# Performance work log

Measured on AMD Instinct MI355X. Metric: run time of the kernel, lower is better.

Reference implementation:

```python
import jax, jax.numpy as jnp
import numpy as np

N, E, IN, H, C, L = 40000, 640000, 256, 128, 64, 4
ALPHA, LAMB = 0.5, 1.0


def setup_inputs() -> dict:
    key = jax.random.key(0)
    ks = jax.random.split(key, 8)
    x = jax.random.normal(ks[0], (N, IN), jnp.float32)
    src = jax.random.randint(ks[1], (E,), 0, N, jnp.int32)
    dst = jax.random.randint(ks[2], (E,), 0, N, jnp.int32)
    s_in = 1.0 / np.sqrt(IN)
    s_h = 1.0 / np.sqrt(H)
    fc1_w = jax.random.normal(ks[3], (IN, H), jnp.float32) * s_in
    fc1_b = jnp.zeros((H,), jnp.float32)
    W1 = jax.random.normal(ks[4], (L, H, H), jnp.float32) * s_h   # GCN2Conv weight1 per layer
    W2 = jax.random.normal(ks[5], (L, H, H), jnp.float32) * s_h   # GCN2Conv weight2 (initial-residual proj)
    bgc = jnp.zeros((L, H), jnp.float32)                          # GCN2Conv bias per layer
    fc2_w = jax.random.normal(ks[6], (H, C), jnp.float32) * s_h
    fc2_b = jnp.zeros((C,), jnp.float32)
    return dict(x=x, fc1_w=fc1_w, fc1_b=fc1_b, W1=W1, W2=W2, bgc=bgc,
                fc2_w=fc2_w, fc2_b=fc2_b, src=src, dst=dst)


def reference(x, fc1_w, fc1_b, W1, W2, bgc, fc2_w, fc2_b, src, dst):
    ones = jnp.ones((E,), x.dtype)
    # symmetric 'both' normalization: deg_out^{-1/2} on src side, deg_in^{-1/2} on dst side
    deg_out = jnp.clip(jax.ops.segment_sum(ones, src, num_segments=N), 1.0)
    deg_in = jnp.clip(jax.ops.segment_sum(ones, dst, num_segments=N), 1.0)
    norm_s = (deg_out ** -0.5)[:, None]
    norm_d = (deg_in ** -0.5)[:, None]

    # feature_preprocess: dropout (eval = identity) -> fc1 -> relu
    h0 = jax.nn.relu(x @ fc1_w + fc1_b)          # [N, H]
    h = h0
    for l in range(L):
        beta = float(np.log(LAMB / (l + 1) + 1.0))
        identity = h
        # sparse neighbor aggregation (SpMM via gather + segment_sum)
        agg = jax.ops.segment_sum((h * norm_s)[src], dst, num_segments=N) * norm_d
        feat = (1.0 - ALPHA) * agg               # smoothed features
        f0 = ALPHA * h0                          # initial residual
        rst = (1.0 - beta) * (feat + f0) + beta * (feat @ W1[l] + f0 @ W2[l]) + bgc[l]
        h = jax.nn.relu(rst + identity)          # outer residual + activation (dropout eval = identity)
    return h @ fc2_w + fc2_b                     # [N, C]
```

## Files before the change

kernel.cpp:

```cpp
#include <hip/hip_runtime.h>
#include <math.h>

#define N_NODES 40000
#define N_EDGES 640000
#define IN_F 256
#define H_F 128
#define C_F 64
#define L_LAYERS 4
#define SCAN_BLKS 157

typedef short short8 __attribute__((ext_vector_type(8)));
typedef unsigned short ushort8 __attribute__((ext_vector_type(8)));
typedef float f32x4 __attribute__((ext_vector_type(4)));

__device__ inline short to_bf16(float f) {
    unsigned u = __builtin_bit_cast(unsigned, f);
    unsigned r = (u + 0x7FFFu + ((u >> 16) & 1u)) >> 16;
    return (short)r;
}
__device__ inline float bf16_to_f(unsigned short u) {
    unsigned v = ((unsigned)u) << 16;
    return __builtin_bit_cast(float, v);
}

__device__ inline int block_excl_scan(int v, int* wsum, int* tot) {
    int tid = threadIdx.x;
    int lane = tid & 63, wid = tid >> 6;
    int incl = v;
    #pragma unroll
    for (int off = 1; off < 64; off <<= 1) {
        int t = __shfl_up(incl, off, 64);
        if (lane >= off) incl += t;
    }
    if (lane == 63) wsum[wid] = incl;
    __syncthreads();
    int prefix = 0, total = 0;
    #pragma unroll
    for (int w = 0; w < 4; w++) {
        int s = wsum[w];
        if (w < wid) prefix += s;
        total += s;
    }
    *tot = total;
    return prefix + incl - v;
}

__global__ void prep_w(const float* __restrict__ fc1_w,
                       const float* __restrict__ W1, const float* __restrict__ W2,
                       const float* __restrict__ fc2_w,
                       short* __restrict__ fc1_wT, short* __restrict__ WcatT,
                       short* __restrict__ fc2_wT) {
    int i = blockIdx.x * 256 + threadIdx.x;
    if (i < 128 * 256) {
        int n = i >> 8, k = i & 255;
        fc1_wT[i] = to_bf16(fc1_w[k * H_F + n]);
    }
    if (i < 4 * 128 * 256) {
        int l = i >> 15; int r = i & 32767; int n = r >> 8; int k = r & 255;
        float w = (k < 128) ? W1[l * 16384 + k * H_F + n]
                            : W2[l * 16384 + (k - 128) * H_F + n];
        WcatT[i] = to_bf16(0.5f * w);
    }
    if (i < 64 * 128) {
        int n = i >> 7, k = i & 127;
        fc2_wT[i] = to_bf16(fc2_w[k * C_F + n]);
    }
}

#define CVT8(dstv, p) {                                                         \
    float4 _v0 = *(const float4*)(p); float4 _v1 = *(const float4*)((p) + 4);   \
    dstv[0] = to_bf16(_v0.x); dstv[1] = to_bf16(_v0.y);                         \
    dstv[2] = to_bf16(_v0.z); dstv[3] = to_bf16(_v0.w);                         \
    dstv[4] = to_bf16(_v1.x); dstv[5] = to_bf16(_v1.y);                         \
    dstv[6] = to_bf16(_v1.z); dstv[7] = to_bf16(_v1.w); }

__global__ __launch_bounds__(256) void deg_fc1_fused(const int* __restrict__ src,
                                                     const int* __restrict__ dst,
                                                     int* __restrict__ cnt_out,
                                                     int* __restrict__ cnt_in,
                                                     unsigned short* __restrict__ pos16,
                                                     const float* __restrict__ x,
                                                     const short* __restrict__ wT,
                                                     const float* __restrict__ b,
                                                     unsigned short* __restrict__ h0b) {
    int blk = blockIdx.x;
    if ((blk & 1) == 0) {
        int e0 = (blk >> 1) * 1024 + threadIdx.x * 4;
        int4 s4 = *(const int4*)(src + e0);
        int4 d4 = *(const int4*)(dst + e0);
        pos16[e0 + 0] = (unsigned short)atomicAdd(&cnt_in[d4.x], 1);
        pos16[e0 + 1] = (unsigned short)atomicAdd(&cnt_in[d4.y], 1);
        pos16[e0 + 2] = (unsigned short)atomicAdd(&cnt_in[d4.z], 1);
        pos16[e0 + 3] = (unsigned short)atomicAdd(&cnt_in[d4.w], 1);
        atomicAdd(&cnt_out[s4.x], 1);
        atomicAdd(&cnt_out[s4.y], 1);
        atomicAdd(&cnt_out[s4.z], 1);
        atomicAdd(&cnt_out[s4.w], 1);
        return;
    }
    int bb = blk >> 1;
    int tid = threadIdx.x;
    int wave = tid >> 6, lane = tid & 63;
    int m = lane & 15, quad = lane >> 4;
    int row = bb * 64 + wave * 16 + m;
    const float* xr = x + (size_t)row * IN_F + quad * 8;
    short8 afrag[8];
    #pragma unroll
    for (int ks = 0; ks < 8; ks++) {
        CVT8(afrag[ks], xr + ks * 32);
    }
    #pragma unroll
    for (int c = 0; c < 8; c += 2) {
        f32x4 acc0 = {0.f, 0.f, 0.f, 0.f};
        f32x4 acc1 = {0.f, 0.f, 0.f, 0.f};
        const short* b0p = wT + (size_t)(c * 16 + m) * IN_F + quad * 8;
        const short* b1p = b0p + 16 * IN_F;
        #pragma unroll
        for (int ks = 0; ks < 8; ks++) {
            short8 b0 = *(const short8*)(b0p + ks * 32);
            short8 b1 = *(const short8*)(b1p + ks * 32);
            acc0 = __builtin_amdgcn_mfma_f32_16x16x32_bf16(afrag[ks], b0, acc0, 0, 0, 0);
            acc1 = __builtin_amdgcn_mfma_f32_16x16x32_bf16(afrag[ks], b1, acc1, 0, 0, 0);
        }
        int col0 = c * 16 + m;
        int rbase = bb * 64 + wave * 16 + quad * 4;
        float bg0 = b[col0], bg1 = b[col0 + 16];
        #pragma unroll
        for (int r = 0; r < 4; r++) {
            size_t idx = (size_t)(rbase + r) * H_F + col0;
            float v0 = acc0[r] + bg0;
            float v1 = acc1[r] + bg1;
            v0 = v0 > 0.f ? v0 : 0.f;
            v1 = v1 > 0.f ? v1 : 0.f;
            h0b[idx] = (unsigned short)to_bf16(v0);
            h0b[idx + 16] = (unsigned short)to_bf16(v1);
        }
    }
}

__global__ __launch_bounds__(256) void scan1(const int* __restrict__ cnt_in,
                                             int* __restrict__ row_local,
                                             int* __restrict__ blk_sum) {
    __shared__ int wsum[4];
    int n = blockIdx.x * 256 + threadIdx.x;
    int v = (n < N_NODES) ? cnt_in[n] : 0;
    int tot;
    int excl = block_excl_scan(v, wsum, &tot);
    if (n < N_NODES) row_local[n] = excl;
    if (threadIdx.x == 0) blk_sum[blockIdx.x] = tot;
}

__global__ __launch_bounds__(256) void scan2(const int* __restrict__ blk_sum,
                                             int* __restrict__ blk_off) {
    __shared__ int wsum[4];
    int t = threadIdx.x;
    int v = (t < SCAN_BLKS) ? blk_sum[t] : 0;
    int tot;
    int excl = block_excl_scan(v, wsum, &tot);
    if (t < SCAN_BLKS) blk_off[t] = excl;
}

__global__ __launch_bounds__(256) void fill_fused(const int* __restrict__ src,
                                                  const int* __restrict__ dst,
                                                  const unsigned short* __restrict__ pos16,
                                                  const int* __restrict__ cnt_out,
                                                  const int* __restrict__ cnt_in,
                                                  const int* __restrict__ row_local,
                                                  const int* __restrict__ blk_off,
                                                  int* __restrict__ col,
                                                  float* __restrict__ wv,
                                                  int* __restrict__ row_ptr) {
    int blk = blockIdx.x;
    if (blk < 2500) {
        int e = blk * 256 + threadIdx.x;
        int s = src[e], d = dst[e];
        int rp = blk_off[d >> 8] + row_local[d] + (int)pos16[e];
        int ds = cnt_out[s]; if (ds < 1) ds = 1;
        int dd = cnt_in[d];  if (dd < 1) dd = 1;
        col[rp] = s;
        wv[rp] = (1.0f / sqrtf((float)ds)) * (1.0f / sqrtf((float)dd));
        return;
    }
    int n = (blk - 2500) * 256 + threadIdx.x;
    if (n < N_NODES) row_ptr[n] = blk_off[n >> 8] + row_local[n];
    if (blk == 2500 && threadIdx.x == 0) row_ptr[N_NODES] = N_EDGES;
}

__global__ __launch_bounds__(256) void spmm_kernel(const unsigned short* __restrict__ hb,
                                                   const int* __restrict__ row_ptr,
                                                   const int* __restrict__ col,
                                                   const float* __restrict__ wv,
                                                   float* __restrict__ agg) {
    int wave = threadIdx.x >> 6, lane = threadIdx.x & 63;
    int slot = lane >> 4, fi = lane & 15;
    int n = blockIdx.x * 4 + wave;
    int e0 = row_ptr[n], e1 = row_ptr[n + 1];
    float a[8] = {};
    int e = e0 + slot;
    for (; e + 12 < e1; e += 16) {
        int c0 = col[e];      float w0 = wv[e];
        int c1 = col[e + 4];  float w1 = wv[e + 4];
        int c2 = col[e + 8];  float w2 = wv[e + 8];
        int c3 = col[e + 12]; float w3 = wv[e + 12];
        ushort8 u0 = *(const ushort8*)(hb + (size_t)c0 * H_F + fi * 8);
        ushort8 u1 = *(const ushort8*)(hb + (size_t)c1 * H_F + fi * 8);
        ushort8 u2 = *(const ushort8*)(hb + (size_t)c2 * H_F + fi * 8);
        ushort8 u3 = *(const ushort8*)(hb + (size_t)c3 * H_F + fi * 8);
        #pragma unroll
        for (int j = 0; j < 8; j++) {
            a[j] += w0 * bf16_to_f(u0[j]) + w1 * bf16_to_f(u1[j])
                  + w2 * bf16_to_f(u2[j]) + w3 * bf16_to_f(u3[j]);
        }
    }
    for (; e < e1; e += 4) {
        int c = col[e];
        float w = wv[e];
        ushort8 u = *(const ushort8*)(hb + (size_t)c * H_F + fi * 8);
        #pragma unroll
        for (int j = 0; j < 8; j++) a[j] += w * bf16_to_f(u[j]);
    }
    #pragma unroll
    for (int mask = 16; mask <= 32; mask <<= 1) {
        #pragma unroll
        for (int j = 0; j < 8; j++) a[j] += __shfl_xor(a[j], mask, 64);
    }
    if (slot == 0) {
        float4* ap = (float4*)(agg + (size_t)n * H_F + fi * 8);
        float4 r0 = {a[0], a[1], a[2], a[3]};
        float4 r1 = {a[4], a[5], a[6], a[7]};
        ap[0] = r0;
        ap[1] = r1;
    }
}

__global__ __launch_bounds__(256) void combine_mfma(const float* __restrict__ agg,
                                                    const unsigned short* __restrict__ h0b,
                                                    const float* __restrict__ h_in_f,
                                                    const unsigned short* __restrict__ h_in_b,
                                                    const short* __restrict__ wT,
                                                    const float* __restrict__ bgc,
                                                    float beta,
                                                    float* __restrict__ h_out,
                                                    unsigned short* __restrict__ h_outb) {
    int tid = threadIdx.x;
    int wave = tid >> 6, lane = tid & 63;
    int m = lane & 15, quad = lane >> 4;
    int row = blockIdx.x * 64 + wave * 16 + m;
    const float* aggr = agg + (size_t)row * H_F + quad * 8;
    const unsigned short* h0r = h0b + (size_t)row * H_F + quad * 8;
    short8 afrag[8];
    #pragma unroll
    for (int ks = 0; ks < 4; ks++) {
        CVT8(afrag[ks], aggr + ks * 32);
    }
    #pragma unroll
    for (int ks = 0; ks < 4; ks++) {
        afrag[ks + 4] = __builtin_bit_cast(short8, *(const ushort8*)(h0r + ks * 32));
    }
    float omb = 1.f - beta;
    #pragma unroll
    for (int c = 0; c < 8; c += 2) {
        f32x4 acc0 = {0.f, 0.f, 0.f, 0.f};
        f32x4 acc1 = {0.f, 0.f, 0.f, 0.f};
        const short* b0p = wT + (size_t)(c * 16 + m) * 256 + quad * 8;
        const short* b1p = b0p + 16 * 256;
        #pragma unroll
        for (int ks = 0; ks < 8; ks++) {
            short8 b0 = *(const short8*)(b0p + ks * 32);
            short8 b1 = *(const short8*)(b1p + ks * 32);
            acc0 = __builtin_amdgcn_mfma_f32_16x16x32_bf16(afrag[ks], b0, acc0, 0, 0, 0);
            acc1 = __builtin_amdgcn_mfma_f32_16x16x32_bf16(afrag[ks], b1, acc1, 0, 0, 0);
        }
        int col0 = c * 16 + m;
        int rbase = blockIdx.x * 64 + wave * 16 + quad * 4;
        float bg0 = bgc[col0], bg1 = bgc[col0 + 16];
        #pragma unroll
        for (int r = 0; r < 4; r++) {
            size_t idx = (size_t)(rbase + r) * H_F + col0;
            float s0 = 0.5f * (agg[idx] + bf16_to_f(h0b[idx]));
            float s1 = 0.5f * (agg[idx + 16] + bf16_to_f(h0b[idx + 16]));
            float id0 = h_in_f ? h_in_f[idx] : bf16_to_f(h_in_b[idx]);
            float id1 = h_in_f ? h_in_f[idx + 16] : bf16_to_f(h_in_b[idx + 16]);
            float v0 = omb * s0 + beta * acc0[r] + bg0 + id0;
            float v1 = omb * s1 + beta * acc1[r] + bg1 + id1;
            v0 = v0 > 0.f ? v0 : 0.f;
            v1 = v1 > 0.f ? v1 : 0.f;
            if (h_out) {
                h_out[idx] = v0;
                h_out[idx + 16] = v1;
            }
            h_outb[idx] = (unsigned short)to_bf16(v0);
            h_outb[idx + 16] = (unsigned short)to_bf16(v1);
        }
    }
}

__global__ __launch_bounds__(256) void fc2_mfma(const unsigned short* __restrict__ hb,
                                                const short* __restrict__ wT,
                                                const float* __restrict__ b,
                                                float* __restrict__ out) {
    int tid = threadIdx.x;
    int wave = tid >> 6, lane = tid & 63;
    int m = lane & 15, quad = lane >> 4;
    int row = blockIdx.x * 64 + wave * 16 + m;
    const unsigned short* hr = hb + (size_t)row * H_F + quad * 8;
    short8 afrag[4];
    #pragma unroll
    for (int ks = 0; ks < 4; ks++) {
        afrag[ks] = __builtin_bit_cast(short8, *(const ushort8*)(hr + ks * 32));
    }
    #pragma unroll
    for (int c = 0; c < 4; c += 2) {
        f32x4 acc0 = {0.f, 0.f, 0.f, 0.f};
        f32x4 acc1 = {0.f, 0.f, 0.f, 0.f};
        const short* b0p = wT + (size_t)(c * 16 + m) * H_F + quad * 8;
        const short* b1p = b0p + 16 * H_F;
        #pragma unroll
        for (int ks = 0; ks < 4; ks++) {
            short8 b0 = *(const short8*)(b0p + ks * 32);
            short8 b1 = *(const short8*)(b1p + ks * 32);
            acc0 = __builtin_amdgcn_mfma_f32_16x16x32_bf16(afrag[ks], b0, acc0, 0, 0, 0);
            acc1 = __builtin_amdgcn_mfma_f32_16x16x32_bf16(afrag[ks], b1, acc1, 0, 0, 0);
        }
        int col0 = c * 16 + m;
        int rbase = blockIdx.x * 64 + wave * 16 + quad * 4;
        float bg0 = b[col0], bg1 = b[col0 + 16];
        #pragma unroll
        for (int r = 0; r < 4; r++) {
            size_t idx = (size_t)(rbase + r) * C_F + col0;
            out[idx] = acc0[r] + bg0;
            out[idx + 16] = acc1[r] + bg1;
        }
    }
}

extern "C" void kernel_launch(void* const* d_in, const int* in_sizes, int n_in,
                              void* d_out, int out_size, void* d_ws, size_t ws_size,
                              hipStream_t stream) {
    const float* x     = (const float*)d_in[0];
    const float* fc1_w = (const float*)d_in[1];
    const float* fc1_b = (const float*)d_in[2];
    const float* W1    = (const float*)d_in[3];
    const float* W2    = (const float*)d_in[4];
    const float* bgc   = (const float*)d_in[5];
    const float* fc2_w = (const float*)d_in[6];
    const float* fc2_b = (const float*)d_in[7];
    const int*   src   = (const int*)d_in[8];
    const int*   dst   = (const int*)d_in[9];
    float* out = (float*)d_out;

    char* p = (char*)d_ws;
    auto alloc = [&](size_t bytes) {
        char* r = p;
        p += (bytes + 255) & ~(size_t)255;
        return r;
    };
    int*   cnt_out   = (int*)alloc((size_t)N_NODES * 4);
    int*   cnt_in    = (int*)alloc((size_t)N_NODES * 4);
    int*   row_ptr   = (int*)alloc((size_t)(N_NODES + 1) * 4);
    int*   row_local = (int*)alloc((size_t)N_NODES * 4);
    int*   blk_sum   = (int*)alloc((size_t)SCAN_BLKS * 4);
    int*   blk_off   = (int*)alloc((size_t)SCAN_BLKS * 4);
    unsigned short* pos16 = (unsigned short*)alloc((size_t)N_EDGES * 2);
    int*   col     = (int*)alloc((size_t)N_EDGES * 4);
    float* wv      = (float*)alloc((size_t)N_EDGES * 4);
    float* hA      = (float*)alloc((size_t)N_NODES * H_F * 4);
    float* hB      = (float*)alloc((size_t)N_NODES * H_F * 4);
    float* agg     = (float*)alloc((size_t)N_NODES * H_F * 4);
    unsigned short* h0b = (unsigned short*)alloc((size_t)N_NODES * H_F * 2);
    unsigned short* hAb = (unsigned short*)alloc((size_t)N_NODES * H_F * 2);
    unsigned short* hBb = (unsigned short*)alloc((size_t)N_NODES * H_F * 2);
    short* fc1_wT  = (short*)alloc((size_t)128 * 256 * 2);
    short* WcatT   = (short*)alloc((size_t)4 * 128 * 256 * 2);
    short* fc2_wT  = (short*)alloc((size_t)64 * 128 * 2);

    hipMemsetAsync(cnt_out, 0, (size_t)N_NODES * 4, stream);
    hipMemsetAsync(cnt_in,  0, (size_t)N_NODES * 4, stream);

    prep_w<<<512, 256, 0, stream>>>(fc1_w, W1, W2, fc2_w, fc1_wT, WcatT, fc2_wT);
    deg_fc1_fused<<<1250, 256, 0, stream>>>(src, dst, cnt_out, cnt_in, pos16,
                                            x, fc1_wT, fc1_b, h0b);
    scan1<<<SCAN_BLKS, 256, 0, stream>>>(cnt_in, row_local, blk_sum);
    scan2<<<1, 256, 0, stream>>>(blk_sum, blk_off);
    fill_fused<<<2500 + SCAN_BLKS, 256, 0, stream>>>(src, dst, pos16, cnt_out, cnt_in,
                                                     row_local, blk_off, col, wv, row_ptr);

    const float* id_f[4]          = {nullptr, hA, hB, hA};
    const unsigned short* id_b    = h0b;
    const unsigned short* sp_in[4]= {h0b, hAb, hBb, hAb};
    float* out_f[4]               = {hA, hB, hA, nullptr};
    unsigned short* out_b[4]      = {hAb, hBb, hAb, hBb};

    for (int l = 0; l < L_LAYERS; l++) {
        float beta = (float)log(1.0 / (double)(l + 1) + 1.0);
        spmm_kernel<<<N_NODES / 4, 256, 0, stream>>>(sp_in[l], row_ptr, col, wv, agg);
        combine_mfma<<<N_NODES / 64, 256, 0, stream>>>(agg, h0b, id_f[l], id_b,
                                                       WcatT + (size_t)l * 128 * 256,
                                                       bgc + (size_t)l * H_F,
                                                       beta, out_f[l], out_b[l]);
    }
    fc2_mfma<<<N_NODES / 64, 256, 0, stream>>>(hBb, fc2_wT, fc2_b, out);
}
```

Baseline: 428.7 us.

## Fuse SpMM into per-layer combine and replace global atomics with chunked LDS histograms

Degree counting and in-edge ranking now use 32 per-chunk LDS histograms with 16-bit packed counters, plus a scan that computes per-chunk bases and reciprocal square-root degrees. This replaces global atomics and the two memsets. Each layer now does the SpMM aggregation into LDS and the MFMA combine in a single kernel, which drops the fp32 agg round trip and the fp32 h copies; the identity term is read from the bf16 hidden state. In exchange, the fused layer launches only 625 blocks, each doing serial per-node gathers, so there is less parallelism to hide gather latency. The packed 16-bit counters and 8-bit local ranks assume per-chunk node degrees stay small.

```diff
diff --git a/kernel.cpp b/kernel.cpp
--- a/kernel.cpp
+++ b/kernel.cpp
@@ -8,6 +8,9 @@
 #define C_F 64
 #define L_LAYERS 4
 #define SCAN_BLKS 157
+#define N_CHUNKS 32
+#define CHUNK_E 20000
+#define LDS_STRIDE 132
 
 typedef short short8 __attribute__((ext_vector_type(8)));
 typedef unsigned short ushort8 __attribute__((ext_vector_type(8)));
@@ -74,31 +77,43 @@
     dstv[4] = to_bf16(_v1.x); dstv[5] = to_bf16(_v1.y);                         \
     dstv[6] = to_bf16(_v1.z); dstv[7] = to_bf16(_v1.w); }
 
-__global__ __launch_bounds__(256) void deg_fc1_fused(const int* __restrict__ src,
-                                                     const int* __restrict__ dst,
-                                                     int* __restrict__ cnt_out,
-                                                     int* __restrict__ cnt_in,
-                                                     unsigned short* __restrict__ pos16,
-                                                     const float* __restrict__ x,
-                                                     const short* __restrict__ wT,
-                                                     const float* __restrict__ b,
-                                                     unsigned short* __restrict__ h0b) {
+__global__ __launch_bounds__(256) void hist_fc1(const int* __restrict__ src,
+                                                const int* __restrict__ dst,
+                                                int* __restrict__ chunk_dst,
+                                                int* __restrict__ chunk_src,
+                                                unsigned char* __restrict__ lrank8,
+                                                const float* __restrict__ x,
+                                                const short* __restrict__ wT,
+                                                const float* __restrict__ b,
+                                                unsigned short* __restrict__ h0b) {
+    __shared__ int cntp[CHUNK_E];
     int blk = blockIdx.x;
-    if ((blk & 1) == 0) {
-        int e0 = (blk >> 1) * 1024 + threadIdx.x * 4;
-        int4 s4 = *(const int4*)(src + e0);
-        int4 d4 = *(const int4*)(dst + e0);
-        pos16[e0 + 0] = (unsigned short)atomicAdd(&cnt_in[d4.x], 1);
-        pos16[e0 + 1] = (unsigned short)atomicAdd(&cnt_in[d4.y], 1);
-        pos16[e0 + 2] = (unsigned short)atomicAdd(&cnt_in[d4.z], 1);
-        pos16[e0 + 3] = (unsigned short)atomicAdd(&cnt_in[d4.w], 1);
-        atomicAdd(&cnt_out[s4.x], 1);
-        atomicAdd(&cnt_out[s4.y], 1);
-        atomicAdd(&cnt_out[s4.z], 1);
-        atomicAdd(&cnt_out[s4.w], 1);
+    if (blk < 64) {
+        int role_dst = (blk < 32);
+        int w = role_dst ? blk : blk - 32;
+        const int* idx = role_dst ? dst : src;
+        int base = w * CHUNK_E;
+        for (int i = threadIdx.x; i < CHUNK_E; i += 256) cntp[i] = 0;
+        __syncthreads();
+        if (role_dst) {
+            for (int i = threadIdx.x; i < CHUNK_E; i += 256) {
+                int d = idx[base + i];
+                int sh = (d & 1) * 16;
+                int old = atomicAdd(&cntp[d >> 1], 1 << sh);
+                lrank8[base + i] = (unsigned char)((old >> sh) & 0xffff);
+            }
+        } else {
+            for (int i = threadIdx.x; i < CHUNK_E; i += 256) {
+                int s = idx[base + i];
+                atomicAdd(&cntp[s >> 1], 1 << ((s & 1) * 16));
+            }
+        }
+        __syncthreads();
+        int* outp = role_dst ? (chunk_dst + w * CHUNK_E) : (chunk_src + w * CHUNK_E);
+        for (int i = threadIdx.x; i < CHUNK_E; i += 256) outp[i] = cntp[i];
         return;
     }
-    int bb = blk >> 1;
+    int bb = blk - 64;
     int tid = threadIdx.x;
     int wave = tid >> 6, lane = tid & 63;
     int m = lane & 15, quad = lane >> 4;
@@ -127,25 +142,46 @@
         float bg0 = b[col0], bg1 = b[col0 + 16];
         #pragma unroll
         for (int r = 0; r < 4; r++) {
-            size_t idx = (size_t)(rbase + r) * H_F + col0;
+            size_t idx2 = (size_t)(rbase + r) * H_F + col0;
             float v0 = acc0[r] + bg0;
             float v1 = acc1[r] + bg1;
             v0 = v0 > 0.f ? v0 : 0.f;
             v1 = v1 > 0.f ? v1 : 0.f;
-            h0b[idx] = (unsigned short)to_bf16(v0);
-            h0b[idx + 16] = (unsigned short)to_bf16(v1);
-        }
-    }
-}
-
-__global__ __launch_bounds__(256) void scan1(const int* __restrict__ cnt_in,
+            h0b[idx2] = (unsigned short)to_bf16(v0);
+            h0b[idx2 + 16] = (unsigned short)to_bf16(v1);
+        }
+    }
+}
+
+__global__ __launch_bounds__(256) void scan1(const int* __restrict__ chunk_dst,
+                                             const int* __restrict__ chunk_src,
+                                             unsigned short* __restrict__ base16,
+                                             float* __restrict__ rsq_in,
+                                             float* __restrict__ rsq_out,
                                              int* __restrict__ row_local,
                                              int* __restrict__ blk_sum) {
     __shared__ int wsum[4];
     int n = blockIdx.x * 256 + threadIdx.x;
-    int v = (n < N_NODES) ? cnt_in[n] : 0;
+    int deg_in = 0;
+    if (n < N_NODES) {
+        int word = n >> 1, sh = (n & 1) * 16;
+        int run = 0;
+        #pragma unroll 4
+        for (int w = 0; w < N_CHUNKS; w++) {
+            int v = (chunk_dst[w * CHUNK_E + word] >> sh) & 0xffff;
+            base16[w * N_NODES + n] = (unsigned short)run;
+            run += v;
+        }
+        deg_in = run;
+        int so = 0;
+        #pragma unroll 4
+        for (int w = 0; w < N_CHUNKS; w++)
+            so += (chunk_src[w * CHUNK_E + word] >> sh) & 0xffff;
+        rsq_in[n] = 1.0f / sqrtf((float)(deg_in < 1 ? 1 : deg_in));
+        rsq_out[n] = 1.0f / sqrtf((float)(so < 1 ? 1 : so));
+    }
     int tot;
-    int excl = block_excl_scan(v, wsum, &tot);
+    int excl = block_excl_scan(deg_in, wsum, &tot);
     if (n < N_NODES) row_local[n] = excl;
     if (threadIdx.x == 0) blk_sum[blockIdx.x] = tot;
 }
@@ -162,23 +198,24 @@
 
 __global__ __launch_bounds__(256) void fill_fused(const int* __restrict__ src,
                                                   const int* __restrict__ dst,
-                                                  const unsigned short* __restrict__ pos16,
-                                                  const int* __restrict__ cnt_out,
-                                                  const int* __restrict__ cnt_in,
+                                                  const unsigned char* __restrict__ lrank8,
+                                                  const unsigned short* __restrict__ base16,
                                                   const int* __restrict__ row_local,
                                                   const int* __restrict__ blk_off,
+                                                  const float* __restrict__ rsq_in,
+                                                  const float* __restrict__ rsq_out,
                                                   int* __restrict__ col,
                                                   float* __restrict__ wv,
                                                   int* __restrict__ row_ptr) {
     int blk = blockIdx.x;
     if (blk < 2500) {
         int e = blk * 256 + threadIdx.x;
+        int w = e / CHUNK_E;
         int s = src[e], d = dst[e];
-        int rp = blk_off[d >> 8] + row_local[d] + (int)pos16[e];
-        int ds = cnt_out[s]; if (ds < 1) ds = 1;
-        int dd = cnt_in[d];  if (dd < 1) dd = 1;
+        int rp = blk_off[d >> 8] + row_local[d] + (int)base16[w * N_NODES + d]
+               + (int)lrank8[e];
         col[rp] = s;
-        wv[rp] = (1.0f / sqrtf((float)ds)) * (1.0f / sqrtf((float)dd));
+        wv[rp] = rsq_out[s] * rsq_in[d];
         return;
     }
     int n = (blk - 2500) * 256 + threadIdx.x;
@@ -186,68 +223,66 @@
     if (blk == 2500 && threadIdx.x == 0) row_ptr[N_NODES] = N_EDGES;
 }
 
-__global__ __launch_bounds__(256) void spmm_kernel(const unsigned short* __restrict__ hb,
+__global__ __launch_bounds__(256) void layer_fused(const unsigned short* __restrict__ hb,
+                                                   const unsigned short* __restrict__ h0b,
                                                    const int* __restrict__ row_ptr,
                                                    const int* __restrict__ col,
                                                    const float* __restrict__ wv,
-                                                   float* __restrict__ agg) {
-    int wave = threadIdx.x >> 6, lane = threadIdx.x & 63;
-    int slot = lane >> 4, fi = lane & 15;
-    int n = blockIdx.x * 4 + wave;
-    int e0 = row_ptr[n], e1 = row_ptr[n + 1];
-    float a[8] = {};
-    int e = e0 + slot;
-    for (; e + 12 < e1; e += 16) {
-        int c0 = col[e];      float w0 = wv[e];
-        int c1 = col[e + 4];  float w1 = wv[e + 4];
-        int c2 = col[e + 8];  float w2 = wv[e + 8];
-        int c3 = col[e + 12]; float w3 = wv[e + 12];
-        ushort8 u0 = *(const ushort8*)(hb + (size_t)c0 * H_F + fi * 8);
-        ushort8 u1 = *(const ushort8*)(hb + (size_t)c1 * H_F + fi * 8);
-        ushort8 u2 = *(const ushort8*)(hb + (size_t)c2 * H_F + fi * 8);
-        ushort8 u3 = *(const ushort8*)(hb + (size_t)c3 * H_F + fi * 8);
-        #pragma unroll
-        for (int j = 0; j < 8; j++) {
-            a[j] += w0 * bf16_to_f(u0[j]) + w1 * bf16_to_f(u1[j])
-                  + w2 * bf16_to_f(u2[j]) + w3 * bf16_to_f(u3[j]);
-        }
-    }
-    for (; e < e1; e += 4) {
-        int c = col[e];
-        float w = wv[e];
-        ushort8 u = *(const ushort8*)(hb + (size_t)c * H_F + fi * 8);
-        #pragma unroll
-        for (int j = 0; j < 8; j++) a[j] += w * bf16_to_f(u[j]);
-    }
-    #pragma unroll
-    for (int mask = 16; mask <= 32; mask <<= 1) {
-        #pragma unroll
-        for (int j = 0; j < 8; j++) a[j] += __shfl_xor(a[j], mask, 64);
-    }
-    if (slot == 0) {
-        float4* ap = (float4*)(agg + (size_t)n * H_F + fi * 8);
-        float4 r0 = {a[0], a[1], a[2], a[3]};
-        float4 r1 = {a[4], a[5], a[6], a[7]};
-        ap[0] = r0;
-        ap[1] = r1;
-    }
-}
-
-__global__ __launch_bounds__(256) void combine_mfma(const float* __restrict__ agg,
-                                                    const unsigned short* __restrict__ h0b,
-                                                    const float* __restrict__ h_in_f,
-                                                    const unsigned short* __restrict__ h_in_b,
-                                                    const short* __restrict__ wT,
-                                                    const float* __restrict__ bgc,
-                                                    float beta,
-                                                    float* __restrict__ h_out,
-                                                    unsigned short* __restrict__ h_outb) {
+                                                   const short* __restrict__ wT,
+                                                   const float* __restrict__ bgc,
+                                                   float beta,
+                                                   unsigned short* __restrict__ h_outb) {
+    __shared__ float aggL[64 * LDS_STRIDE];
     int tid = threadIdx.x;
     int wave = tid >> 6, lane = tid & 63;
+    int slot = lane >> 4, fi = lane & 15;
+    int nodebase = blockIdx.x * 64 + wave * 16;
+
+    for (int i = 0; i < 16; i++) {
+        int n = nodebase + i;
+        int e0 = row_ptr[n], e1 = row_ptr[n + 1];
+        float a[8] = {};
+        int e = e0 + slot;
+        for (; e + 12 < e1; e += 16) {
+            int c0 = col[e];      float w0 = wv[e];
+            int c1 = col[e + 4];  float w1 = wv[e + 4];
+            int c2 = col[e + 8];  float w2 = wv[e + 8];
+            int c3 = col[e + 12]; float w3 = wv[e + 12];
+            ushort8 u0 = *(const ushort8*)(hb + (size_t)c0 * H_F + fi * 8);
+            ushort8 u1 = *(const ushort8*)(hb + (size_t)c1 * H_F + fi * 8);
+            ushort8 u2 = *(const ushort8*)(hb + (size_t)c2 * H_F + fi * 8);
+            ushort8 u3 = *(const ushort8*)(hb + (size_t)c3 * H_F + fi * 8);
+            #pragma unroll
+            for (int j = 0; j < 8; j++) {
+                a[j] += w0 * bf16_to_f(u0[j]) + w1 * bf16_to_f(u1[j])
+                      + w2 * bf16_to_f(u2[j]) + w3 * bf16_to_f(u3[j]);
+            }
+        }
+        for (; e < e1; e += 4) {
+            int c = col[e];
+            float w = wv[e];
+            ushort8 u = *(const ushort8*)(hb + (size_t)c * H_F + fi * 8);
+            #pragma unroll
+            for (int j = 0; j < 8; j++) a[j] += w * bf16_to_f(u[j]);
+        }
+        #pragma unroll
+        for (int mask = 16; mask <= 32; mask <<= 1) {
+            #pragma unroll
+            for (int j = 0; j < 8; j++) a[j] += __shfl_xor(a[j], mask, 64);
+        }
+        if (slot == 0) {
+            float* ap = aggL + (wave * 16 + i) * LDS_STRIDE + fi * 8;
+            float4 r0 = {a[0], a[1], a[2], a[3]};
+            float4 r1 = {a[4], a[5], a[6], a[7]};
+            *(float4*)ap = r0;
+            *(float4*)(ap + 4) = r1;
+        }
+    }
+    __syncthreads();
+
     int m = lane & 15, quad = lane >> 4;
-    int row = blockIdx.x * 64 + wave * 16 + m;
-    const float* aggr = agg + (size_t)row * H_F + quad * 8;
-    const unsigned short* h0r = h0b + (size_t)row * H_F + quad * 8;
+    const float* aggr = aggL + (wave * 16 + m) * LDS_STRIDE + quad * 8;
+    const unsigned short* h0r = h0b + (size_t)(nodebase + m) * H_F + quad * 8;
     short8 afrag[8];
     #pragma unroll
     for (int ks = 0; ks < 4; ks++) {
@@ -272,23 +307,18 @@
             acc1 = __builtin_amdgcn_mfma_f32_16x16x32_bf16(afrag[ks], b1, acc1, 0, 0, 0);
         }
         int col0 = c * 16 + m;
-        int rbase = blockIdx.x * 64 + wave * 16 + quad * 4;
-        float bg0 = bgc[col0], bg1 = bgc[col0 + 16];
+        int rl = wave * 16 + quad * 4;
         #pragma unroll
         for (int r = 0; r < 4; r++) {
-            size_t idx = (size_t)(rbase + r) * H_F + col0;
-            float s0 = 0.5f * (agg[idx] + bf16_to_f(h0b[idx]));
-            float s1 = 0.5f * (agg[idx + 16] + bf16_to_f(h0b[idx + 16]));
-            float id0 = h_in_f ? h_in_f[idx] : bf16_to_f(h_in_b[idx]);
-            float id1 = h_in_f ? h_in_f[idx + 16] : bf16_to_f(h_in_b[idx + 16]);
-            float v0 = omb * s0 + beta * acc0[r] + bg0 + id0;
-            float v1 = omb * s1 + beta * acc1[r] + bg1 + id1;
+            size_t idx = (size_t)(nodebase + quad * 4 + r) * H_F + col0;
+            float ag0 = aggL[(rl + r) * LDS_STRIDE + col0];
+            float ag1 = aggL[(rl + r) * LDS_STRIDE + col0 + 16];
+            float s0 = 0.5f * (ag0 + bf16_to_f(h0b[idx]));
+            float s1 = 0.5f * (ag1 + bf16_to_f(h0b[idx + 16]));
+            float v0 = omb * s0 + beta * acc0[r] + bgc[col0] + bf16_to_f(hb[idx]);
+            float v1 = omb * s1 + beta * acc1[r] + bgc[col0 + 16] + bf16_to_f(hb[idx + 16]);
             v0 = v0 > 0.f ? v0 : 0.f;
             v1 = v1 > 0.f ? v1 : 0.f;
-            if (h_out) {
-                h_out[idx] = v0;
-                h_out[idx + 16] = v1;
-            }
             h_outb[idx] = (unsigned short)to_bf16(v0);
             h_outb[idx + 16] = (unsigned short)to_bf16(v1);
         }
@@ -355,18 +385,18 @@
         p += (bytes + 255) & ~(size_t)255;
         return r;
     };
-    int*   cnt_out   = (int*)alloc((size_t)N_NODES * 4);
-    int*   cnt_in    = (int*)alloc((size_t)N_NODES * 4);
+    int*   chunk_dst = (int*)alloc((size_t)N_CHUNKS * CHUNK_E * 4);
+    int*   chunk_src = (int*)alloc((size_t)N_CHUNKS * CHUNK_E * 4);
+    unsigned short* base16 = (unsigned short*)alloc((size_t)N_CHUNKS * N_NODES * 2);
+    unsigned char*  lrank8 = (unsigned char*)alloc((size_t)N_EDGES);
+    float* rsq_in  = (float*)alloc((size_t)N_NODES * 4);
+    float* rsq_out = (float*)alloc((size_t)N_NODES * 4);
     int*   row_ptr   = (int*)alloc((size_t)(N_NODES + 1) * 4);
     int*   row_local = (int*)alloc((size_t)N_NODES * 4);
     int*   blk_sum   = (int*)alloc((size_t)SCAN_BLKS * 4);
     int*   blk_off   = (int*)alloc((size_t)SCAN_BLKS * 4);
-    unsigned short* pos16 = (unsigned short*)alloc((size_t)N_EDGES * 2);
     int*   col     = (int*)alloc((size_t)N_EDGES * 4);
     float* wv      = (float*)alloc((size_t)N_EDGES * 4);
-    float* hA      = (float*)alloc((size_t)N_NODES * H_F * 4);
-    float* hB      = (float*)alloc((size_t)N_NODES * H_F * 4);
-    float* agg     = (float*)alloc((size_t)N_NODES * H_F * 4);
     unsigned short* h0b = (unsigned short*)alloc((size_t)N_NODES * H_F * 2);
     unsigned short* hAb = (unsigned short*)alloc((size_t)N_NODES * H_F * 2);
     unsigned short* hBb = (unsigned short*)alloc((size_t)N_NODES * H_F * 2);
@@ -374,30 +404,24 @@
     short* WcatT   = (short*)alloc((size_t)4 * 128 * 256 * 2);
     short* fc2_wT  = (short*)alloc((size_t)64 * 128 * 2);
 
-    hipMemsetAsync(cnt_out, 0, (size_t)N_NODES * 4, stream);
-    hipMemsetAsync(cnt_in,  0, (size_t)N_NODES * 4, stream);
-
     prep_w<<<512, 256, 0, stream>>>(fc1_w, W1, W2, fc2_w, fc1_wT, WcatT, fc2_wT);
-    deg_fc1_fused<<<1250, 256, 0, stream>>>(src, dst, cnt_out, cnt_in, pos16,
-                                            x, fc1_wT, fc1_b, h0b);
-    scan1<<<SCAN_BLKS, 256, 0, stream>>>(cnt_in, row_local, blk_sum);
+    hist_fc1<<<689, 256, 0, stream>>>(src, dst, chunk_dst, chunk_src, lrank8,
+                                      x, fc1_wT, fc1_b, h0b);
+    scan1<<<SCAN_BLKS, 256, 0, stream>>>(chunk_dst, chunk_src, base16,
+                                         rsq_in, rsq_out, row_local, blk_sum);
     scan2<<<1, 256, 0, stream>>>(blk_sum, blk_off);
-    fill_fused<<<2500 + SCAN_BLKS, 256, 0, stream>>>(src, dst, pos16, cnt_out, cnt_in,
-                                                     row_local, blk_off, col, wv, row_ptr);
-
-    const float* id_f[4]          = {nullptr, hA, hB, hA};
-    const unsigned short* id_b    = h0b;
-    const unsigned short* sp_in[4]= {h0b, hAb, hBb, hAb};
-    float* out_f[4]               = {hA, hB, hA, nullptr};
-    unsigned short* out_b[4]      = {hAb, hBb, hAb, hBb};
-
+    fill_fused<<<2500 + SCAN_BLKS, 256, 0, stream>>>(src, dst, lrank8, base16,
+                                                     row_local, blk_off, rsq_in, rsq_out,
+                                                     col, wv, row_ptr);
+
+    const unsigned short* sp_in[4] = {h0b, hAb, hBb, hAb};
+    unsigned short* out_b[4]       = {hAb, hBb, hAb, hBb};
     for (int l = 0; l < L_LAYERS; l++) {
         float beta = (float)log(1.0 / (double)(l + 1) + 1.0);
-        spmm_kernel<<<N_NODES / 4, 256, 0, stream>>>(sp_in[l], row_ptr, col, wv, agg);
-        combine_mfma<<<N_NODES / 64, 256, 0, stream>>>(agg, h0b, id_f[l], id_b,
-                                                       WcatT + (size_t)l * 128 * 256,
-                                                       bgc + (size_t)l * H_F,
-                                                       beta, out_f[l], out_b[l]);
+        layer_fused<<<N_NODES / 64, 256, 0, stream>>>(sp_in[l], h0b, row_ptr, col, wv,
+                                                      WcatT + (size_t)l * 128 * 256,
+                                                      bgc + (size_t)l * H_F,
+                                                      beta, out_b[l]);
     }
     fc2_mfma<<<N_NODES / 64, 256, 0, stream>>>(hBb, fc2_wT, fc2_b, out);
 }
```

After: 465.6 us. +8.6%, slower.
